# Optimization experiments

Measured on AMD Instinct MI355X. Metric: run time of the kernel, lower is better.

## Reference

```python
import jax, jax.numpy as jnp
import numpy as np

D_MODEL = 1024
NHEAD = 16


def setup_inputs() -> dict:
    key = jax.random.key(0)
    ks = jax.random.split(key, 11)
    B, T, D = 2, 2048, D_MODEL
    s = 1.0 / np.sqrt(D)
    inp = {
        "query": jax.random.normal(ks[0], (B, T, D), jnp.float32),
        "key_": jax.random.normal(ks[1], (B, T, D), jnp.float32),
        "value": jax.random.normal(ks[2], (B, T, D), jnp.float32),
        "q_w": jax.random.uniform(ks[3], (D, D), jnp.float32, -s, s),
        "q_b": jax.random.uniform(ks[4], (D,), jnp.float32, -s, s),
        "k_w": jax.random.uniform(ks[5], (D, D), jnp.float32, -s, s),
        "k_b": jax.random.uniform(ks[6], (D,), jnp.float32, -s, s),
        "v_w": jax.random.uniform(ks[7], (D, D), jnp.float32, -s, s),
        "v_b": jax.random.uniform(ks[8], (D,), jnp.float32, -s, s),
        "o_w": jax.random.uniform(ks[9], (D, D), jnp.float32, -s, s),
        "o_b": jax.random.uniform(ks[10], (D,), jnp.float32, -s, s),
    }
    return inp


def reference(query, key_, value, q_w, q_b, k_w, k_b, v_w, v_b, o_w, o_b):
    B, T, D = query.shape
    H = NHEAD
    dh = D // H
    # Linear projections (torch nn.Linear: x @ W.T + b)
    q = (query @ q_w.T + q_b).reshape(B, T, H, dh).transpose(0, 2, 1, 3)
    k = (key_ @ k_w.T + k_b).reshape(B, T, H, dh).transpose(0, 2, 1, 3)
    v = (value @ v_w.T + v_b).reshape(B, T, H, dh).transpose(0, 2, 1, 3)
    # scaled dot-product scores [B,H,T,T]
    scores = jnp.einsum("bhqd,bhkd->bhqk", q, k) / jnp.sqrt(jnp.float32(dh))
    # causal mask (mask is not None branch in the original)
    causal = jnp.triu(jnp.ones((T, T), dtype=bool), k=1)
    scores = jnp.where(causal, jnp.float32(-jnp.inf), scores)
    w = jax.nn.softmax(scores, axis=-1)
    out = jnp.einsum("bhqk,bhkd->bhqd", w, v)
    out = out.transpose(0, 2, 1, 3).reshape(B, T, D)
    return out @ o_w.T + o_b
```

## Files before the change

### kernel.cpp

```cpp
#include <hip/hip_runtime.h>
#include <hip/hip_bf16.h>

using bf16 = __hip_bfloat16;
typedef __attribute__((ext_vector_type(8))) short short8;
typedef __attribute__((ext_vector_type(4))) float floatx4;

#define DEVINL __device__ __forceinline__

constexpr int NHEAD = 16;
constexpr int DH = 64;
constexpr int T_ = 2048;
constexpr int DM = 1024;
constexpr float LOG2E = 1.44269504088896340736f;

typedef const __attribute__((address_space(1))) unsigned int* gas1_t;
typedef __attribute__((address_space(3))) unsigned int* las3_t;

DEVINL void async_cp16(void* lds, const void* g) {
  __builtin_amdgcn_global_load_lds((gas1_t)g, (las3_t)lds, 16, 0, 0);
}

DEVINL void wave_wait_dma() {
  __builtin_amdgcn_s_waitcnt(0x0F70);
  __builtin_amdgcn_sched_barrier(0);
}

struct alignas(8) bf4 { bf16 x, y, z, w; };

DEVINL unsigned pack2(float a, float b) {
  union { bf16 h[2]; unsigned u; } x;
  x.h[0] = __float2bfloat16(a);
  x.h[1] = __float2bfloat16(b);
  return x.u;
}

struct CvtArgs { const float* src[7]; bf16* dst[7]; };

__global__ __launch_bounds__(256) void cvt_kernel(CvtArgs a) {
  const int total = 3 * 1048576 + 4 * 262144;
  for (int i = blockIdx.x * 256 + threadIdx.x; i < total; i += gridDim.x * 256) {
    int t, off;
    if (i < 3 * 1048576) { t = i >> 20; off = i & 1048575; }
    else { int j = i - 3 * 1048576; t = 3 + (j >> 18); off = j & 262143; }
    float4 v = ((const float4*)a.src[t])[off];
    bf4 o;
    o.x = __float2bfloat16(v.x); o.y = __float2bfloat16(v.y);
    o.z = __float2bfloat16(v.z); o.w = __float2bfloat16(v.w);
    ((bf4*)a.dst[t])[off] = o;
  }
}

template <int EPI, int JT>
DEVINL void gemm_body(const bf16* __restrict__ A, const bf16* __restrict__ W,
                      const float* __restrict__ bias, void* __restrict__ out,
                      float scale, int vmode, int row0, int col0) {
  constexpr int K = 1024;
  constexpr int BN = JT * 32;
  __shared__ bf16 As[128 * 32];
  __shared__ bf16 Bs[BN * 32];
  const int tid = threadIdx.x;
  const int lane = tid & 63, l16 = lane & 15, quad = lane >> 4;
  const int wave = tid >> 6;
  const int wm = (wave & 1) << 6, wn = (wave >> 1) * (JT * 16);

  floatx4 acc[4][JT];
#pragma unroll
  for (int i = 0; i < 4; ++i)
#pragma unroll
    for (int j = 0; j < JT; ++j) acc[i][j] = (floatx4){0.f, 0.f, 0.f, 0.f};

  const int r0 = tid >> 2, c0 = (tid & 3) ^ (r0 & 3);
  const int t1 = tid + 256;
  const int r1 = t1 >> 2, c1 = (t1 & 3) ^ (r1 & 3);

  for (int kt = 0; kt < K / 32; ++kt) {
    const int k0 = kt * 32;
    async_cp16(As + tid * 8, A + (size_t)(row0 + r0) * K + k0 + c0 * 8);
    async_cp16(As + t1 * 8,  A + (size_t)(row0 + r1) * K + k0 + c1 * 8);
    async_cp16(Bs + tid * 8, W + (size_t)(col0 + r0) * K + k0 + c0 * 8);
    if (BN == 128)
      async_cp16(Bs + t1 * 8, W + (size_t)(col0 + r1) * K + k0 + c1 * 8);
    __syncthreads();
    short8 af[4], bfr[JT];
#pragma unroll
    for (int i = 0; i < 4; ++i) {
      int r = wm + i * 16 + l16;
      af[i] = *(const short8*)(As + (r * 4 + (quad ^ (r & 3))) * 8);
    }
#pragma unroll
    for (int j = 0; j < JT; ++j) {
      int r = wn + j * 16 + l16;
      bfr[j] = *(const short8*)(Bs + (r * 4 + (quad ^ (r & 3))) * 8);
    }
#pragma unroll
    for (int i = 0; i < 4; ++i)
#pragma unroll
      for (int j = 0; j < JT; ++j)
        acc[i][j] = __builtin_amdgcn_mfma_f32_16x16x32_bf16(af[i], bfr[j], acc[i][j], 0, 0, 0);
    __syncthreads();
  }

#pragma unroll
  for (int j = 0; j < JT; ++j) {
    const int col = col0 + wn + j * 16 + l16;
    const float bv = bias[col];
#pragma unroll
    for (int i = 0; i < 4; ++i) {
      const int m0 = row0 + wm + i * 16 + quad * 4;
      if (EPI == 1) {
#pragma unroll
        for (int r = 0; r < 4; ++r)
          ((float*)out)[(size_t)(m0 + r) * DM + col] = acc[i][j][r] + bv;
      } else if (vmode) {
        const int b = m0 >> 11, t = m0 & 2047, h = col >> 6, d = col & 63;
        bf4 o;
        o.x = __float2bfloat16((acc[i][j][0] + bv) * scale);
        o.y = __float2bfloat16((acc[i][j][1] + bv) * scale);
        o.z = __float2bfloat16((acc[i][j][2] + bv) * scale);
        o.w = __float2bfloat16((acc[i][j][3] + bv) * scale);
        *(bf4*)((bf16*)out + (((size_t)(b * NHEAD + h)) * DH + d) * T_ + t) = o;
      } else {
#pragma unroll
        for (int r = 0; r < 4; ++r) {
          const int m = m0 + r;
          const int b = m >> 11, t = m & 2047, h = col >> 6, d = col & 63;
          ((bf16*)out)[(((size_t)(b * NHEAD + h)) * T_ + t) * DH + d] =
              __float2bfloat16((acc[i][j][r] + bv) * scale);
        }
      }
    }
  }
}

struct GemmBatch {
  const bf16* A[3]; const bf16* W[3]; const float* bias[3];
  bf16* out[3]; float scale[3]; int vmode[3];
};

__global__ __launch_bounds__(256, 2) void qkv_gemm(GemmBatch p) {
  const int g = blockIdx.z;
  gemm_body<0, 4>(p.A[g], p.W[g], p.bias[g], p.out[g], p.scale[g], p.vmode[g],
                  blockIdx.y * 128, blockIdx.x * 128);
}

__global__ __launch_bounds__(256, 2) void out_gemm(const bf16* __restrict__ A,
                                                   const bf16* __restrict__ W,
                                                   const float* __restrict__ bias,
                                                   float* __restrict__ out) {
  gemm_body<1, 2>(A, W, bias, out, 1.0f, 0, blockIdx.y * 128, blockIdx.x * 64);
}

__global__ __launch_bounds__(128, 2)
void attn_kernel(const bf16* __restrict__ Q, const bf16* __restrict__ Kg_,
                 const bf16* __restrict__ Vt, bf16* __restrict__ Og) {
  const int qt = (blockIdx.x + blockIdx.y) & 31;
  const int bh = blockIdx.y;
  const int q0 = qt * 64;
  const int tid = threadIdx.x, lane = tid & 63, wave = tid >> 6;
  const int quad = lane >> 4, l16 = lane & 15;

  __shared__ bf16 smem[2][2][4096];
  __shared__ float lx[64];

  const bf16* Kp = Kg_ + (size_t)bh * T_ * DH;
  const bf16* Vp = Vt + (size_t)bh * DH * T_;
  const bf16* Qp = Q + ((size_t)bh * T_ + q0) * DH;

  short8 qf[4][2];
#pragma unroll
  for (int qi = 0; qi < 4; ++qi)
#pragma unroll
    for (int kk = 0; kk < 2; ++kk)
      qf[qi][kk] = *(const short8*)(Qp + (size_t)(qi * 16 + l16) * DH + kk * 32 + quad * 8);

  floatx4 Oa[4][4];
  float l_r[4];
#pragma unroll
  for (int qi = 0; qi < 4; ++qi) {
#pragma unroll
    for (int td = 0; td < 4; ++td) Oa[qi][td] = (floatx4){0.f, 0.f, 0.f, 0.f};
    l_r[qi] = 0.f;
  }

  const int ntiles = 2 * (qt + 1);

  {
    const int kt2 = wave;
#pragma unroll
    for (int i = 0; i < 4; ++i) {
      int t = lane + i * 64;
      int rk = t >> 3, ck = (t & 7) ^ (rk & 7);
      async_cp16(&smem[wave][0][t * 8], Kp + (size_t)(kt2 * 32 + rk) * DH + ck * 8);
      int rv = t >> 2, cv = (t & 3) ^ (rv & 3);
      async_cp16(&smem[wave][0][2048 + t * 8], Vp + (size_t)rv * T_ + kt2 * 32 + cv * 8);
    }
  }

  for (int kt2 = wave, buf = 0; kt2 < ntiles; kt2 += 2, buf ^= 1) {
    const bf16* Ks = &smem[wave][buf][0];
    const bf16* Vs = &smem[wave][buf][2048];

    wave_wait_dma();
    short8 kf[2][2], vf[4];
#pragma unroll
    for (int kk = 0; kk < 2; ++kk)
#pragma unroll
      for (int tj = 0; tj < 2; ++tj) {
        int r = tj * 16 + l16;
        int cg = kk * 4 + quad;
        kf[kk][tj] = *(const short8*)(Ks + (r * 8 + (cg ^ (r & 7))) * 8);
      }
#pragma unroll
    for (int td = 0; td < 4; ++td) {
      int r = td * 16 + l16;
      vf[td] = *(const short8*)(Vs + (r * 4 + (quad ^ (r & 3))) * 8);
    }

    if (kt2 + 2 < ntiles) {
#pragma unroll
      for (int i = 0; i < 4; ++i) {
        int t = lane + i * 64;
        int rk = t >> 3, ck = (t & 7) ^ (rk & 7);
        async_cp16(&smem[wave][buf ^ 1][t * 8],
                   Kp + (size_t)((kt2 + 2) * 32 + rk) * DH + ck * 8);
        int rv = t >> 2, cv = (t & 3) ^ (rv & 3);
        async_cp16(&smem[wave][buf ^ 1][2048 + t * 8],
                   Vp + (size_t)rv * T_ + (kt2 + 2) * 32 + cv * 8);
      }
    }

    floatx4 S[4][2];
#pragma unroll
    for (int qi = 0; qi < 4; ++qi)
#pragma unroll
      for (int tj = 0; tj < 2; ++tj) S[qi][tj] = (floatx4){0.f, 0.f, 0.f, 0.f};
#pragma unroll
    for (int kk = 0; kk < 2; ++kk)
#pragma unroll
      for (int tj = 0; tj < 2; ++tj)
#pragma unroll
        for (int qi = 0; qi < 4; ++qi)
          S[qi][tj] = __builtin_amdgcn_mfma_f32_16x16x32_bf16(kf[kk][tj], qf[qi][kk],
                                                              S[qi][tj], 0, 0, 0);

    if (kt2 >= 2 * qt) {
#pragma unroll
      for (int qi = 0; qi < 4; ++qi) {
        const int q = q0 + qi * 16 + l16;
#pragma unroll
        for (int tj = 0; tj < 2; ++tj)
#pragma unroll
          for (int r = 0; r < 4; ++r) {
            int key = kt2 * 32 + tj * 16 + quad * 4 + r;
            if (key > q) S[qi][tj][r] = -3.0e38f;
          }
      }
    }

    unsigned lo[4][2], hi[4][2];
#pragma unroll
    for (int qi = 0; qi < 4; ++qi) {
#pragma unroll
      for (int tj = 0; tj < 2; ++tj)
#pragma unroll
        for (int r = 0; r < 4; ++r)
          S[qi][tj][r] = __builtin_amdgcn_exp2f(S[qi][tj][r]);
      l_r[qi] += ((S[qi][0][0] + S[qi][0][1]) + (S[qi][0][2] + S[qi][0][3])) +
                 ((S[qi][1][0] + S[qi][1][1]) + (S[qi][1][2] + S[qi][1][3]));
#pragma unroll
      for (int tj = 0; tj < 2; ++tj) {
        lo[qi][tj] = pack2(S[qi][tj][0], S[qi][tj][1]);
        hi[qi][tj] = pack2(S[qi][tj][2], S[qi][tj][3]);
      }
    }

    const int sl0 = l16 + ((lane & 16) << 1);
    const int sl1 = sl0 + 16;
    const bool sel = (quad >> 1) != 0;
#pragma unroll
    for (int qi = 0; qi < 4; ++qi) {
      unsigned a0 = __shfl((int)lo[qi][0], sl0), b0 = __shfl((int)lo[qi][1], sl0);
      unsigned a1 = __shfl((int)hi[qi][0], sl0), b1 = __shfl((int)hi[qi][1], sl0);
      unsigned a2 = __shfl((int)lo[qi][0], sl1), b2 = __shfl((int)lo[qi][1], sl1);
      unsigned a3 = __shfl((int)hi[qi][0], sl1), b3 = __shfl((int)hi[qi][1], sl1);
      union { unsigned u[4]; short8 v; } pfu;
      pfu.u[0] = sel ? b0 : a0;
      pfu.u[1] = sel ? b1 : a1;
      pfu.u[2] = sel ? b2 : a2;
      pfu.u[3] = sel ? b3 : a3;
#pragma unroll
      for (int td = 0; td < 4; ++td)
        Oa[qi][td] = __builtin_amdgcn_mfma_f32_16x16x32_bf16(vf[td], pfu.v, Oa[qi][td], 0, 0, 0);
    }
  }

#pragma unroll
  for (int qi = 0; qi < 4; ++qi) {
    l_r[qi] += __shfl_xor(l_r[qi], 16);
    l_r[qi] += __shfl_xor(l_r[qi], 32);
  }

  if (wave == 1) {
    float* cb = (float*)&smem[1][0][0];
#pragma unroll
    for (int qi = 0; qi < 4; ++qi) {
#pragma unroll
      for (int td = 0; td < 4; ++td)
        ((floatx4*)cb)[(qi * 4 + td) * 64 + lane] = Oa[qi][td];
      if (quad == 0) lx[qi * 16 + l16] = l_r[qi];
    }
  }
  __syncthreads();
  if (wave == 0) {
    const float* cb = (const float*)&smem[1][0][0];
    const int b = bh >> 4, h = bh & 15;
#pragma unroll
    for (int qi = 0; qi < 4; ++qi) {
      const int q = q0 + qi * 16 + l16;
      const float rl = __builtin_amdgcn_rcpf(l_r[qi] + lx[qi * 16 + l16]);
      bf16* op = Og + ((size_t)(b * T_ + q)) * DM + h * DH + quad * 4;
#pragma unroll
      for (int td = 0; td < 4; ++td) {
        floatx4 p = ((const floatx4*)cb)[(qi * 4 + td) * 64 + lane];
        bf4 o;
        o.x = __float2bfloat16((Oa[qi][td][0] + p[0]) * rl);
        o.y = __float2bfloat16((Oa[qi][td][1] + p[1]) * rl);
        o.z = __float2bfloat16((Oa[qi][td][2] + p[2]) * rl);
        o.w = __float2bfloat16((Oa[qi][td][3] + p[3]) * rl);
        *(bf4*)(op + td * 16) = o;
      }
    }
  }
}

extern "C" void kernel_launch(void* const* d_in, const int* in_sizes, int n_in,
                              void* d_out, int out_size, void* d_ws, size_t ws_size,
                              hipStream_t stream) {
  (void)in_sizes; (void)n_in; (void)out_size; (void)ws_size;
  const float* query = (const float*)d_in[0];
  const float* key_  = (const float*)d_in[1];
  const float* value = (const float*)d_in[2];
  const float* q_w = (const float*)d_in[3];
  const float* q_b = (const float*)d_in[4];
  const float* k_w = (const float*)d_in[5];
  const float* k_b = (const float*)d_in[6];
  const float* v_w = (const float*)d_in[7];
  const float* v_b = (const float*)d_in[8];
  const float* o_w = (const float*)d_in[9];
  const float* o_b = (const float*)d_in[10];

  char* ws = (char*)d_ws;
  const size_t MB = (size_t)1 << 20;
  bf16* Xq = (bf16*)(ws + 0 * MB);
  bf16* Xk = (bf16*)(ws + 8 * MB);
  bf16* Xv = (bf16*)(ws + 16 * MB);
  bf16* Wq = (bf16*)(ws + 24 * MB);
  bf16* Wk = (bf16*)(ws + 26 * MB);
  bf16* Wv = (bf16*)(ws + 28 * MB);
  bf16* Wo = (bf16*)(ws + 30 * MB);
  bf16* Qb = (bf16*)(ws + 32 * MB);
  bf16* Kb = (bf16*)(ws + 40 * MB);
  bf16* Vt = (bf16*)(ws + 48 * MB);
  bf16* An = (bf16*)(ws + 64 * MB);

  CvtArgs ca;
  ca.src[0] = query; ca.src[1] = key_; ca.src[2] = value;
  ca.src[3] = q_w; ca.src[4] = k_w; ca.src[5] = v_w; ca.src[6] = o_w;
  ca.dst[0] = Xq; ca.dst[1] = Xk; ca.dst[2] = Xv;
  ca.dst[3] = Wq; ca.dst[4] = Wk; ca.dst[5] = Wv; ca.dst[6] = Wo;
  cvt_kernel<<<2048, 256, 0, stream>>>(ca);

  GemmBatch gb;
  gb.A[0] = Xq; gb.A[1] = Xk; gb.A[2] = Xv;
  gb.W[0] = Wq; gb.W[1] = Wk; gb.W[2] = Wv;
  gb.bias[0] = q_b; gb.bias[1] = k_b; gb.bias[2] = v_b;
  gb.out[0] = Qb; gb.out[1] = Kb; gb.out[2] = Vt;
  gb.scale[0] = 0.125f * LOG2E; gb.scale[1] = 1.f; gb.scale[2] = 1.f;
  gb.vmode[0] = 0; gb.vmode[1] = 0; gb.vmode[2] = 1;
  qkv_gemm<<<dim3(8, 32, 3), 256, 0, stream>>>(gb);

  attn_kernel<<<dim3(32, 32), 128, 0, stream>>>(Qb, Kb, Vt, An);
  out_gemm<<<dim3(16, 32), 256, 0, stream>>>(An, Wo, o_b, (float*)d_out);
}
```

Baseline: 225.3 us.

## Pair causal query tiles per block and split keys across four waves

The attention kernel now runs 4 waves per block instead of 2. Each block handles two query tiles (qp and 31-qp) in sequence, so every block gets the same total amount of causal work. Keys are split four ways across the waves, and the partial outputs and row sums are combined through LDS, with each wave normalizing and writing 16 rows. This targets the load imbalance of causal attention and the short key loops on early tiles. In exchange it adds a larger cross-wave reduction, an extra block barrier, and more LDS per block, which may reduce occupancy.

```diff
diff --git a/kernel.cpp b/kernel.cpp
--- a/kernel.cpp
+++ b/kernel.cpp
@@ -150,186 +150,193 @@
   gemm_body<1, 2>(A, W, bias, out, 1.0f, 0, blockIdx.y * 128, blockIdx.x * 64);
 }
 
-__global__ __launch_bounds__(128, 2)
+__global__ __launch_bounds__(256, 2)
 void attn_kernel(const bf16* __restrict__ Q, const bf16* __restrict__ Kg_,
                  const bf16* __restrict__ Vt, bf16* __restrict__ Og) {
-  const int qt = (blockIdx.x + blockIdx.y) & 31;
+  const int qp = blockIdx.x;
   const int bh = blockIdx.y;
-  const int q0 = qt * 64;
   const int tid = threadIdx.x, lane = tid & 63, wave = tid >> 6;
   const int quad = lane >> 4, l16 = lane & 15;
 
-  __shared__ bf16 smem[2][2][4096];
-  __shared__ float lx[64];
+  __shared__ bf16 tiles[4][2][4096];
+  __shared__ float lx[4][64];
 
   const bf16* Kp = Kg_ + (size_t)bh * T_ * DH;
   const bf16* Vp = Vt + (size_t)bh * DH * T_;
-  const bf16* Qp = Q + ((size_t)bh * T_ + q0) * DH;
-
-  short8 qf[4][2];
-#pragma unroll
-  for (int qi = 0; qi < 4; ++qi)
-#pragma unroll
-    for (int kk = 0; kk < 2; ++kk)
-      qf[qi][kk] = *(const short8*)(Qp + (size_t)(qi * 16 + l16) * DH + kk * 32 + quad * 8);
-
-  floatx4 Oa[4][4];
-  float l_r[4];
-#pragma unroll
-  for (int qi = 0; qi < 4; ++qi) {
-#pragma unroll
-    for (int td = 0; td < 4; ++td) Oa[qi][td] = (floatx4){0.f, 0.f, 0.f, 0.f};
-    l_r[qi] = 0.f;
-  }
-
-  const int ntiles = 2 * (qt + 1);
-
-  {
-    const int kt2 = wave;
-#pragma unroll
-    for (int i = 0; i < 4; ++i) {
-      int t = lane + i * 64;
-      int rk = t >> 3, ck = (t & 7) ^ (rk & 7);
-      async_cp16(&smem[wave][0][t * 8], Kp + (size_t)(kt2 * 32 + rk) * DH + ck * 8);
-      int rv = t >> 2, cv = (t & 3) ^ (rv & 3);
-      async_cp16(&smem[wave][0][2048 + t * 8], Vp + (size_t)rv * T_ + kt2 * 32 + cv * 8);
-    }
-  }
-
-  for (int kt2 = wave, buf = 0; kt2 < ntiles; kt2 += 2, buf ^= 1) {
-    const bf16* Ks = &smem[wave][buf][0];
-    const bf16* Vs = &smem[wave][buf][2048];
-
-    wave_wait_dma();
-    short8 kf[2][2], vf[4];
-#pragma unroll
-    for (int kk = 0; kk < 2; ++kk)
-#pragma unroll
-      for (int tj = 0; tj < 2; ++tj) {
-        int r = tj * 16 + l16;
-        int cg = kk * 4 + quad;
-        kf[kk][tj] = *(const short8*)(Ks + (r * 8 + (cg ^ (r & 7))) * 8);
-      }
-#pragma unroll
-    for (int td = 0; td < 4; ++td) {
-      int r = td * 16 + l16;
-      vf[td] = *(const short8*)(Vs + (r * 4 + (quad ^ (r & 3))) * 8);
-    }
-
-    if (kt2 + 2 < ntiles) {
+  const bf16* Qbase = Q + (size_t)bh * T_ * DH;
+  const int b = bh >> 4, h = bh & 15;
+
+#pragma unroll
+  for (int phase = 0; phase < 2; ++phase) {
+    const int qt = phase ? (31 - qp) : qp;
+    const int q0 = qt * 64;
+    const int ntiles = 2 * (qt + 1);
+    const bf16* Qp = Qbase + (size_t)q0 * DH;
+
+    short8 qf[4][2];
+#pragma unroll
+    for (int qi = 0; qi < 4; ++qi)
+#pragma unroll
+      for (int kk = 0; kk < 2; ++kk)
+        qf[qi][kk] = *(const short8*)(Qp + (size_t)(qi * 16 + l16) * DH + kk * 32 + quad * 8);
+
+    floatx4 Oa[4][4];
+    float l_r[4];
+#pragma unroll
+    for (int qi = 0; qi < 4; ++qi) {
+#pragma unroll
+      for (int td = 0; td < 4; ++td) Oa[qi][td] = (floatx4){0.f, 0.f, 0.f, 0.f};
+      l_r[qi] = 0.f;
+    }
+
+    if (wave < ntiles) {
 #pragma unroll
       for (int i = 0; i < 4; ++i) {
         int t = lane + i * 64;
         int rk = t >> 3, ck = (t & 7) ^ (rk & 7);
-        async_cp16(&smem[wave][buf ^ 1][t * 8],
-                   Kp + (size_t)((kt2 + 2) * 32 + rk) * DH + ck * 8);
+        async_cp16(&tiles[wave][0][t * 8], Kp + (size_t)(wave * 32 + rk) * DH + ck * 8);
         int rv = t >> 2, cv = (t & 3) ^ (rv & 3);
-        async_cp16(&smem[wave][buf ^ 1][2048 + t * 8],
-                   Vp + (size_t)rv * T_ + (kt2 + 2) * 32 + cv * 8);
-      }
-    }
-
-    floatx4 S[4][2];
-#pragma unroll
-    for (int qi = 0; qi < 4; ++qi)
-#pragma unroll
-      for (int tj = 0; tj < 2; ++tj) S[qi][tj] = (floatx4){0.f, 0.f, 0.f, 0.f};
-#pragma unroll
-    for (int kk = 0; kk < 2; ++kk)
-#pragma unroll
-      for (int tj = 0; tj < 2; ++tj)
-#pragma unroll
-        for (int qi = 0; qi < 4; ++qi)
-          S[qi][tj] = __builtin_amdgcn_mfma_f32_16x16x32_bf16(kf[kk][tj], qf[qi][kk],
-                                                              S[qi][tj], 0, 0, 0);
-
-    if (kt2 >= 2 * qt) {
+        async_cp16(&tiles[wave][0][2048 + t * 8], Vp + (size_t)rv * T_ + wave * 32 + cv * 8);
+      }
+    }
+
+    int buf = 0;
+    for (int kt2 = wave; kt2 < ntiles; kt2 += 4, buf ^= 1) {
+      const bf16* Ks = &tiles[wave][buf][0];
+      const bf16* Vs = &tiles[wave][buf][2048];
+
+      wave_wait_dma();
+      short8 kf[2][2], vf[4];
+#pragma unroll
+      for (int kk = 0; kk < 2; ++kk)
+#pragma unroll
+        for (int tj = 0; tj < 2; ++tj) {
+          int r = tj * 16 + l16;
+          int cg = kk * 4 + quad;
+          kf[kk][tj] = *(const short8*)(Ks + (r * 8 + (cg ^ (r & 7))) * 8);
+        }
+#pragma unroll
+      for (int td = 0; td < 4; ++td) {
+        int r = td * 16 + l16;
+        vf[td] = *(const short8*)(Vs + (r * 4 + (quad ^ (r & 3))) * 8);
+      }
+
+      if (kt2 + 4 < ntiles) {
+#pragma unroll
+        for (int i = 0; i < 4; ++i) {
+          int t = lane + i * 64;
+          int rk = t >> 3, ck = (t & 7) ^ (rk & 7);
+          async_cp16(&tiles[wave][buf ^ 1][t * 8],
+                     Kp + (size_t)((kt2 + 4) * 32 + rk) * DH + ck * 8);
+          int rv = t >> 2, cv = (t & 3) ^ (rv & 3);
+          async_cp16(&tiles[wave][buf ^ 1][2048 + t * 8],
+                     Vp + (size_t)rv * T_ + (kt2 + 4) * 32 + cv * 8);
+        }
+      }
+
+      floatx4 S[4][2];
+#pragma unroll
+      for (int qi = 0; qi < 4; ++qi)
+#pragma unroll
+        for (int tj = 0; tj < 2; ++tj) S[qi][tj] = (floatx4){0.f, 0.f, 0.f, 0.f};
+#pragma unroll
+      for (int kk = 0; kk < 2; ++kk)
+#pragma unroll
+        for (int tj = 0; tj < 2; ++tj)
+#pragma unroll
+          for (int qi = 0; qi < 4; ++qi)
+            S[qi][tj] = __builtin_amdgcn_mfma_f32_16x16x32_bf16(kf[kk][tj], qf[qi][kk],
+                                                                S[qi][tj], 0, 0, 0);
+
+      if (kt2 >= 2 * qt) {
+#pragma unroll
+        for (int qi = 0; qi < 4; ++qi) {
+          const int q = q0 + qi * 16 + l16;
+#pragma unroll
+          for (int tj = 0; tj < 2; ++tj)
+#pragma unroll
+            for (int r = 0; r < 4; ++r) {
+              int key = kt2 * 32 + tj * 16 + quad * 4 + r;
+              if (key > q) S[qi][tj][r] = -3.0e38f;
+            }
+        }
+      }
+
+      unsigned lo[4][2], hi[4][2];
 #pragma unroll
       for (int qi = 0; qi < 4; ++qi) {
-        const int q = q0 + qi * 16 + l16;
 #pragma unroll
         for (int tj = 0; tj < 2; ++tj)
 #pragma unroll
-          for (int r = 0; r < 4; ++r) {
-            int key = kt2 * 32 + tj * 16 + quad * 4 + r;
-            if (key > q) S[qi][tj][r] = -3.0e38f;
-          }
-      }
-    }
-
-    unsigned lo[4][2], hi[4][2];
+          for (int r = 0; r < 4; ++r)
+            S[qi][tj][r] = __builtin_amdgcn_exp2f(S[qi][tj][r]);
+        l_r[qi] += ((S[qi][0][0] + S[qi][0][1]) + (S[qi][0][2] + S[qi][0][3])) +
+                   ((S[qi][1][0] + S[qi][1][1]) + (S[qi][1][2] + S[qi][1][3]));
+#pragma unroll
+        for (int tj = 0; tj < 2; ++tj) {
+          lo[qi][tj] = pack2(S[qi][tj][0], S[qi][tj][1]);
+          hi[qi][tj] = pack2(S[qi][tj][2], S[qi][tj][3]);
+        }
+      }
+
+      const int sl0 = l16 + ((lane & 16) << 1);
+      const int sl1 = sl0 + 16;
+      const bool sel = (quad >> 1) != 0;
+#pragma unroll
+      for (int qi = 0; qi < 4; ++qi) {
+        unsigned a0 = __shfl((int)lo[qi][0], sl0), b0 = __shfl((int)lo[qi][1], sl0);
+        unsigned a1 = __shfl((int)hi[qi][0], sl0), b1 = __shfl((int)hi[qi][1], sl0);
+        unsigned a2 = __shfl((int)lo[qi][0], sl1), b2 = __shfl((int)lo[qi][1], sl1);
+        unsigned a3 = __shfl((int)hi[qi][0], sl1), b3 = __shfl((int)hi[qi][1], sl1);
+        union { unsigned u[4]; short8 v; } pfu;
+        pfu.u[0] = sel ? b0 : a0;
+        pfu.u[1] = sel ? b1 : a1;
+        pfu.u[2] = sel ? b2 : a2;
+        pfu.u[3] = sel ? b3 : a3;
+#pragma unroll
+        for (int td = 0; td < 4; ++td)
+          Oa[qi][td] = __builtin_amdgcn_mfma_f32_16x16x32_bf16(vf[td], pfu.v, Oa[qi][td], 0, 0, 0);
+      }
+    }
+
 #pragma unroll
     for (int qi = 0; qi < 4; ++qi) {
-#pragma unroll
-      for (int tj = 0; tj < 2; ++tj)
-#pragma unroll
-        for (int r = 0; r < 4; ++r)
-          S[qi][tj][r] = __builtin_amdgcn_exp2f(S[qi][tj][r]);
-      l_r[qi] += ((S[qi][0][0] + S[qi][0][1]) + (S[qi][0][2] + S[qi][0][3])) +
-                 ((S[qi][1][0] + S[qi][1][1]) + (S[qi][1][2] + S[qi][1][3]));
-#pragma unroll
-      for (int tj = 0; tj < 2; ++tj) {
-        lo[qi][tj] = pack2(S[qi][tj][0], S[qi][tj][1]);
-        hi[qi][tj] = pack2(S[qi][tj][2], S[qi][tj][3]);
-      }
-    }
-
-    const int sl0 = l16 + ((lane & 16) << 1);
-    const int sl1 = sl0 + 16;
-    const bool sel = (quad >> 1) != 0;
-#pragma unroll
-    for (int qi = 0; qi < 4; ++qi) {
-      unsigned a0 = __shfl((int)lo[qi][0], sl0), b0 = __shfl((int)lo[qi][1], sl0);
-      unsigned a1 = __shfl((int)hi[qi][0], sl0), b1 = __shfl((int)hi[qi][1], sl0);
-      unsigned a2 = __shfl((int)lo[qi][0], sl1), b2 = __shfl((int)lo[qi][1], sl1);
-      unsigned a3 = __shfl((int)hi[qi][0], sl1), b3 = __shfl((int)hi[qi][1], sl1);
-      union { unsigned u[4]; short8 v; } pfu;
-      pfu.u[0] = sel ? b0 : a0;
-      pfu.u[1] = sel ? b1 : a1;
-      pfu.u[2] = sel ? b2 : a2;
-      pfu.u[3] = sel ? b3 : a3;
-#pragma unroll
-      for (int td = 0; td < 4; ++td)
-        Oa[qi][td] = __builtin_amdgcn_mfma_f32_16x16x32_bf16(vf[td], pfu.v, Oa[qi][td], 0, 0, 0);
-    }
-  }
-
-#pragma unroll
-  for (int qi = 0; qi < 4; ++qi) {
-    l_r[qi] += __shfl_xor(l_r[qi], 16);
-    l_r[qi] += __shfl_xor(l_r[qi], 32);
-  }
-
-  if (wave == 1) {
-    float* cb = (float*)&smem[1][0][0];
+      l_r[qi] += __shfl_xor(l_r[qi], 16);
+      l_r[qi] += __shfl_xor(l_r[qi], 32);
+    }
+
+    float* cb = (float*)&tiles[wave][0][0];
 #pragma unroll
     for (int qi = 0; qi < 4; ++qi) {
 #pragma unroll
       for (int td = 0; td < 4; ++td)
         ((floatx4*)cb)[(qi * 4 + td) * 64 + lane] = Oa[qi][td];
-      if (quad == 0) lx[qi * 16 + l16] = l_r[qi];
-    }
-  }
-  __syncthreads();
-  if (wave == 0) {
-    const float* cb = (const float*)&smem[1][0][0];
-    const int b = bh >> 4, h = bh & 15;
-#pragma unroll
-    for (int qi = 0; qi < 4; ++qi) {
-      const int q = q0 + qi * 16 + l16;
-      const float rl = __builtin_amdgcn_rcpf(l_r[qi] + lx[qi * 16 + l16]);
-      bf16* op = Og + ((size_t)(b * T_ + q)) * DM + h * DH + quad * 4;
+      if (quad == 0) lx[wave][qi * 16 + l16] = l_r[qi];
+    }
+    __syncthreads();
+
+    {
+      const float lsum = lx[0][wave * 16 + l16] + lx[1][wave * 16 + l16] +
+                         lx[2][wave * 16 + l16] + lx[3][wave * 16 + l16];
+      const float rl = __builtin_amdgcn_rcpf(lsum);
+      bf16* op = Og + ((size_t)(b * T_ + q0 + wave * 16 + l16)) * DM + h * DH + quad * 4;
 #pragma unroll
       for (int td = 0; td < 4; ++td) {
-        floatx4 p = ((const floatx4*)cb)[(qi * 4 + td) * 64 + lane];
+        floatx4 s = (floatx4){0.f, 0.f, 0.f, 0.f};
+#pragma unroll
+        for (int src = 0; src < 4; ++src) {
+          floatx4 p = ((const floatx4*)&tiles[src][0][0])[(wave * 4 + td) * 64 + lane];
+          s[0] += p[0]; s[1] += p[1]; s[2] += p[2]; s[3] += p[3];
+        }
         bf4 o;
-        o.x = __float2bfloat16((Oa[qi][td][0] + p[0]) * rl);
-        o.y = __float2bfloat16((Oa[qi][td][1] + p[1]) * rl);
-        o.z = __float2bfloat16((Oa[qi][td][2] + p[2]) * rl);
-        o.w = __float2bfloat16((Oa[qi][td][3] + p[3]) * rl);
+        o.x = __float2bfloat16(s[0] * rl);
+        o.y = __float2bfloat16(s[1] * rl);
+        o.z = __float2bfloat16(s[2] * rl);
+        o.w = __float2bfloat16(s[3] * rl);
         *(bf4*)(op + td * 16) = o;
       }
     }
+    if (phase == 0) __syncthreads();
   }
 }
 
@@ -379,6 +386,6 @@
   gb.vmode[0] = 0; gb.vmode[1] = 0; gb.vmode[2] = 1;
   qkv_gemm<<<dim3(8, 32, 3), 256, 0, stream>>>(gb);
 
-  attn_kernel<<<dim3(32, 32), 128, 0, stream>>>(Qb, Kb, Vt, An);
+  attn_kernel<<<dim3(16, 32), 256, 0, stream>>>(Qb, Kb, Vt, An);
   out_gemm<<<dim3(16, 32), 256, 0, stream>>>(An, Wo, o_b, (float*)d_out);
 }
```

Result: no change. 222.5 us (-1.2%).
